# Kernel tuning notes

Hardware: AMD Instinct MI355X
Metric: run time of the kernel (lower is better)

## Reference

```python
import jax, jax.numpy as jnp
import numpy as np

B, T, D, H = 4, 2048, 1024, 16
HD = D // H  # head_dim = 64
SCALE = HD ** -0.5


def setup_inputs() -> dict:
    key = jax.random.key(0)
    k1, k2, k3 = jax.random.split(key, 3)
    x = jax.random.normal(k1, (B, T, D), dtype=jnp.float32)
    # xavier-uniform-like scaling for weights
    qkv_w = jax.random.normal(k2, (3 * D, D), dtype=jnp.float32) * (2.0 / (4 * D)) ** 0.5
    out_w = jax.random.normal(k3, (D, D), dtype=jnp.float32) * (1.0 / D) ** 0.5
    out_b = jnp.zeros((D,), dtype=jnp.float32)
    return {"x": x, "qkv_w": qkv_w, "out_w": out_w, "out_b": out_b}


def reference(x, qkv_w, out_w, out_b):
    Bx, Tx, _ = x.shape
    # qkv projection (nn.Linear: x @ W^T), no bias
    qkv = jnp.einsum('btd,ed->bte', x, qkv_w)  # [B,T,3D]
    qkv = qkv.reshape(Bx, Tx, 3, H, HD).transpose(2, 0, 3, 1, 4)  # [3,B,H,T,hd]
    q, k, v = qkv[0], qkv[1], qkv[2]
    scores = jnp.einsum('bhqd,bhkd->bhqk', q, k) * SCALE  # [B,H,T,T]
    causal = jnp.triu(jnp.ones((Tx, Tx), dtype=bool), k=1)
    scores = jnp.where(causal, -jnp.inf, scores)
    weights = jax.nn.softmax(scores, axis=-1)
    out = jnp.einsum('bhqk,bhkd->bhqd', weights, v)  # [B,H,T,hd]
    out = out.transpose(0, 2, 1, 3).reshape(Bx, Tx, D)
    return jnp.einsum('btd,ed->bte', out, out_w) + out_b
```

## Files before the change

### kernel.cpp

```cpp
#include <hip/hip_runtime.h>
#include <stdint.h>


typedef __bf16 bfx8 __attribute__((ext_vector_type(8)));
typedef float f32x4 __attribute__((ext_vector_type(4)));
typedef float f32x16 __attribute__((ext_vector_type(16)));

__device__ __forceinline__ uint16_t f2b(float f) {
  uint32_t u = __float_as_uint(f);
  u += 0x7fff + ((u >> 16) & 1);
  return (uint16_t)(u >> 16);
}

__device__ __forceinline__ uint32_t cvt_pk(float lo, float hi) {
  uint32_t r;
  asm("v_cvt_pk_bf16_f32 %0, %1, %2" : "=v"(r) : "v"(lo), "v"(hi));
  return r;
}

__device__ __forceinline__ void gld16(const void* g, void* l) {
  __builtin_amdgcn_global_load_lds((const __attribute__((address_space(1))) void*)g,
                                   (__attribute__((address_space(3))) void*)l,
                                   16, 0, 0);
}

__global__ __launch_bounds__(256) void cvt_bf16(const float* __restrict__ in,
                                                uint16_t* __restrict__ out, int n8) {
  int i = blockIdx.x * 256 + threadIdx.x;
  if (i >= n8) return;
  float4 a = ((const float4*)in)[2 * i];
  float4 b = ((const float4*)in)[2 * i + 1];
  union { uint16_t u[8]; uint4 v; } pk;
  pk.u[0] = f2b(a.x); pk.u[1] = f2b(a.y); pk.u[2] = f2b(a.z); pk.u[3] = f2b(a.w);
  pk.u[4] = f2b(b.x); pk.u[5] = f2b(b.y); pk.u[6] = f2b(b.z); pk.u[7] = f2b(b.w);
  ((uint4*)out)[i] = pk.v;
}

template <int OUTF32>
__global__ __launch_bounds__(256) void gemm_bt(const uint16_t* __restrict__ A,
                                               const uint16_t* __restrict__ B,
                                               void* __restrict__ Cout,
                                               const float* __restrict__ bias,
                                               int M, int N, int K, int nbx, int nwg) {
  __shared__ alignas(16) uint16_t As[2][128 * 32];
  __shared__ alignas(16) uint16_t Bs[2][128 * 32];

  int did = blockIdx.x;
  int wg = (did & 7) * (nwg >> 3) + (did >> 3);
  int bx = wg % nbx, by = wg / nbx;
  int m0 = by * 128, n0 = bx * 128;

  int tid = threadIdx.x;
  int lane = tid & 63, wid = tid >> 6;
  int wm = wid >> 1, wn = wid & 1;

  int rs = wid * 16 + (lane >> 2);
  int cs = (lane & 3) * 8;

  f32x4 acc[4][4] = {};

  auto stage = [&](int buf, int kt) {
    int k0 = kt * 32;
    gld16(&A[(size_t)(m0 + rs) * K + k0 + cs],      &As[buf][wid * 512]);
    gld16(&A[(size_t)(m0 + rs + 64) * K + k0 + cs], &As[buf][wid * 512 + 2048]);
    gld16(&B[(size_t)(n0 + rs) * K + k0 + cs],      &Bs[buf][wid * 512]);
    gld16(&B[(size_t)(n0 + rs + 64) * K + k0 + cs], &Bs[buf][wid * 512 + 2048]);
  };

  stage(0, 0);
  __syncthreads();

  int nk = K >> 5;
  int cur = 0;
  int ko = (lane >> 4) * 8;
  for (int kt = 0; kt < nk; ++kt) {
    if (kt + 1 < nk) stage(cur ^ 1, kt + 1);
    bfx8 a[4], b[4];
#pragma unroll
    for (int mi = 0; mi < 4; ++mi)
      a[mi] = *(const bfx8*)&As[cur][(wm * 64 + mi * 16 + (lane & 15)) * 32 + ko];
#pragma unroll
    for (int ni = 0; ni < 4; ++ni)
      b[ni] = *(const bfx8*)&Bs[cur][(wn * 64 + ni * 16 + (lane & 15)) * 32 + ko];
#pragma unroll
    for (int mi = 0; mi < 4; ++mi)
#pragma unroll
      for (int ni = 0; ni < 4; ++ni)
        acc[mi][ni] =
            __builtin_amdgcn_mfma_f32_16x16x32_bf16(a[mi], b[ni], acc[mi][ni], 0, 0, 0);
    __syncthreads();
    cur ^= 1;
  }

#pragma unroll
  for (int mi = 0; mi < 4; ++mi) {
    int row = m0 + wm * 64 + mi * 16 + ((lane >> 4) << 2);
#pragma unroll
    for (int ni = 0; ni < 4; ++ni) {
      int col = n0 + wn * 64 + ni * 16 + (lane & 15);
#pragma unroll
      for (int r = 0; r < 4; ++r) {
        float v = acc[mi][ni][r];
        if (OUTF32)
          ((float*)Cout)[(size_t)(row + r) * N + col] = v + bias[col];
        else
          ((uint16_t*)Cout)[(size_t)(row + r) * N + col] = f2b(v);
      }
    }
  }
}

__global__ __launch_bounds__(256, 2) void flash_attn(const uint16_t* __restrict__ qkv,
                                                     uint16_t* __restrict__ attnb) {
  const int T = 2048, D3 = 3072;
  const float CSC = 0.125f * 1.44269504f;
  __shared__ alignas(16) uint16_t Ks[3][64 * 64];
  __shared__ alignas(16) uint16_t Vt[3][64 * 64];

  int d = blockIdx.x;
  int bh = d & 63;
  int a = d >> 6;
  int b = bh >> 4, h = bh & 15;

  int tid = threadIdx.x, lane = tid & 63, wid = tid >> 6;
  int l31 = lane & 31, hi = lane >> 5;
  int swz = (lane & 7) << 3;

  size_t base = (size_t)b * T * D3;
  int hoff = h * 64;
  const uint16_t* kbase = &qkv[base + 1024 + hoff];
  const uint16_t* vbase = &qkv[base + 2048 + hoff];

  int krow = wid * 16 + (lane >> 3);
  int kc = ((lane & 7) << 3) ^ ((krow & 7) << 3);
  int vr = (tid & 31) * 2;
  int vc = (tid >> 5) * 8;

  for (int p = 0; p < 2; ++p) {
    int qb = (p == 0) ? (15 - a) : a;
    int q0 = qb << 7;
    int qw = q0 + wid * 32;
    int ntile = 2 * qb + 2;

    float mC = -1e30f, l_r = 0.f;
    f32x16 acc0 = {}, acc1 = {};
    bfx8 pf[4];
    int smax_prev = -1, vb_prev = 0;

    bfx8 qf[4];
    {
      const uint16_t* qp = &qkv[base + (size_t)(qw + l31) * D3 + hoff + 8 * hi];
#pragma unroll
      for (int h4 = 0; h4 < 4; ++h4) qf[h4] = *(const bfx8*)(qp + 16 * h4);
    }

    uint4 vA0, vA1, vB0, vB1;

    auto loadV = [&](int kv0, uint4& r0, uint4& r1) {
      r0 = *(const uint4*)&vbase[(size_t)(kv0 + vr) * D3 + vc];
      r1 = *(const uint4*)&vbase[(size_t)(kv0 + vr + 1) * D3 + vc];
    };
    auto stageK = [&](int buf, int kv0) {
      gld16(&kbase[(size_t)(kv0 + krow) * D3 + kc], &Ks[buf][wid * 1024]);
      gld16(&kbase[(size_t)(kv0 + krow + 8) * D3 + kc], &Ks[buf][wid * 1024 + 512]);
    };
    auto writeV = [&](int vb, const uint4& r0, const uint4& r1) {
      union { uint4 v; uint16_t u[8]; } x, y;
      x.v = r0; y.v = r1;
#pragma unroll
      for (int j = 0; j < 8; ++j) {
        int hd = vc + j;
        uint32_t pk = (uint32_t)x.u[j] | ((uint32_t)y.u[j] << 16);
        *(uint32_t*)&Vt[vb][hd * 64 + (vr ^ ((hd & 7) << 3))] = pk;
      }
    };
    auto doPV = [&]() {
      const uint16_t* vp = &Vt[vb_prev][0];
      __builtin_amdgcn_s_setprio(1);
#pragma unroll
      for (int s = 0; s < 4; ++s) {
        if (s <= smax_prev) {
          bfx8 v0 = *(const bfx8*)&vp[l31 * 64 + ((16 * s + 8 * hi) ^ swz)];
          acc0 = __builtin_amdgcn_mfma_f32_32x32x16_bf16(v0, pf[s], acc0, 0, 0, 0);
          bfx8 v1 = *(const bfx8*)&vp[(32 + l31) * 64 + ((16 * s + 8 * hi) ^ swz)];
          acc1 = __builtin_amdgcn_mfma_f32_32x32x16_bf16(v1, pf[s], acc1, 0, 0, 0);
        }
      }
      __builtin_amdgcn_s_setprio(0);
    };

    loadV(0, vA0, vA1);
    stageK(0, 0);
    writeV(0, vA0, vA1);
    loadV(64, vB0, vB1);
    stageK(1, 64);
    asm volatile("s_waitcnt vmcnt(0) lgkmcnt(0)" ::: "memory");
    __builtin_amdgcn_s_barrier();
    __builtin_amdgcn_sched_barrier(0);

    auto subiter = [&](int t, uint4& f0, uint4& f1, uint4& c0, uint4& c1) {
      int kv0 = t << 6;
      bool issue = (t + 2 < ntile);
      if (issue) {
        loadV((t + 2) << 6, f0, f1);
        stageK((t + 2) % 3, (t + 2) << 6);
      }
      bool active = (kv0 <= qw);
      int tmax = (qw > kv0) ? 2 : 1;
      f32x16 st0 = {}, st1 = {};
      if (active) {
        const uint16_t* kp = &Ks[t % 3][0];
        __builtin_amdgcn_s_setprio(1);
#pragma unroll
        for (int h4 = 0; h4 < 4; ++h4) {
          bfx8 kf0 = *(const bfx8*)&kp[l31 * 64 + ((16 * h4 + 8 * hi) ^ swz)];
          st0 = __builtin_amdgcn_mfma_f32_32x32x16_bf16(kf0, qf[h4], st0, 0, 0, 0);
          if (tmax == 2) {
            bfx8 kf1 = *(const bfx8*)&kp[(32 + l31) * 64 + ((16 * h4 + 8 * hi) ^ swz)];
            st1 = __builtin_amdgcn_mfma_f32_32x32x16_bf16(kf1, qf[h4], st1, 0, 0, 0);
          }
        }
        __builtin_amdgcn_s_setprio(0);
      }

      if (smax_prev >= 0) { doPV(); smax_prev = -1; }

      if (active) {
        int q = qw + l31;
        float mx0 = -1e30f, mx1 = -1e30f;
        if (kv0 == qw) {
#pragma unroll
          for (int r = 0; r < 16; ++r) {
            int kv = kv0 + (r & 3) + 8 * (r >> 2) + 4 * hi;
            float v = st0[r];
            if (kv > q) v = -1e30f;
            st0[r] = v;
            mx0 = fmaxf(mx0, v);
          }
        } else {
#pragma unroll
          for (int r = 0; r < 16; ++r) mx0 = fmaxf(mx0, st0[r]);
        }
        if (tmax == 2) {
          if (kv0 + 32 == qw) {
#pragma unroll
            for (int r = 0; r < 16; ++r) {
              int kv = kv0 + 32 + (r & 3) + 8 * (r >> 2) + 4 * hi;
              float v = st1[r];
              if (kv > q) v = -1e30f;
              st1[r] = v;
              mx1 = fmaxf(mx1, v);
            }
          } else {
#pragma unroll
            for (int r = 0; r < 16; ++r) mx1 = fmaxf(mx1, st1[r]);
          }
        }
        float mS = fmaxf(mx0, mx1) * CSC;
        if (!__all(mS - mC <= 8.0f)) {
          float mSp = fmaxf(mS, __shfl_xor(mS, 32));
          float mCn = fmaxf(mC, mSp);
          float fac = __builtin_amdgcn_exp2f(mC - mCn);
          mC = mCn;
          l_r *= fac;
          acc0 *= fac;
          acc1 *= fac;
        }
        float l0 = 0.f, l1 = 0.f, l2 = 0.f, l3 = 0.f;
#pragma unroll
        for (int r = 0; r < 16; r += 4) {
          float e0 = __builtin_amdgcn_exp2f(fmaf(st0[r], CSC, -mC));
          float e1 = __builtin_amdgcn_exp2f(fmaf(st0[r + 1], CSC, -mC));
          float e2 = __builtin_amdgcn_exp2f(fmaf(st0[r + 2], CSC, -mC));
          float e3 = __builtin_amdgcn_exp2f(fmaf(st0[r + 3], CSC, -mC));
          st0[r] = e0; st0[r + 1] = e1; st0[r + 2] = e2; st0[r + 3] = e3;
          l0 += e0; l1 += e1; l2 += e2; l3 += e3;
        }
        if (tmax == 2) {
#pragma unroll
          for (int r = 0; r < 16; r += 4) {
            float e0 = __builtin_amdgcn_exp2f(fmaf(st1[r], CSC, -mC));
            float e1 = __builtin_amdgcn_exp2f(fmaf(st1[r + 1], CSC, -mC));
            float e2 = __builtin_amdgcn_exp2f(fmaf(st1[r + 2], CSC, -mC));
            float e3 = __builtin_amdgcn_exp2f(fmaf(st1[r + 3], CSC, -mC));
            st1[r] = e0; st1[r + 1] = e1; st1[r + 2] = e2; st1[r + 3] = e3;
            l0 += e0; l1 += e1; l2 += e2; l3 += e3;
          }
        }
        l_r += (l0 + l1) + (l2 + l3);

        int smax = (qw + 31 - kv0) >> 4;
        if (smax > 3) smax = 3;
#pragma unroll
        for (int s = 0; s < 4; ++s) {
          if (s <= smax) {
            int pb = 8 * (s & 1);
            uint32_t W0, W1, W2, W3;
            if (s < 2) {
              W0 = cvt_pk(st0[pb + 0], st0[pb + 1]);
              W1 = cvt_pk(st0[pb + 2], st0[pb + 3]);
              W2 = cvt_pk(st0[pb + 4], st0[pb + 5]);
              W3 = cvt_pk(st0[pb + 6], st0[pb + 7]);
            } else {
              W0 = cvt_pk(st1[pb + 0], st1[pb + 1]);
              W1 = cvt_pk(st1[pb + 2], st1[pb + 3]);
              W2 = cvt_pk(st1[pb + 4], st1[pb + 5]);
              W3 = cvt_pk(st1[pb + 6], st1[pb + 7]);
            }
            auto rA = __builtin_amdgcn_permlane32_swap(W0, W2, false, false);
            auto rB = __builtin_amdgcn_permlane32_swap(W1, W3, false, false);
            union { uint32_t u[4]; bfx8 v; } pk;
            pk.u[0] = rA[0]; pk.u[1] = rB[0]; pk.u[2] = rA[1]; pk.u[3] = rB[1];
            pf[s] = pk.v;
          }
        }
        smax_prev = smax;
        vb_prev = t % 3;
      }

      if (t + 1 < ntile) writeV((t + 1) % 3, c0, c1);

      if (issue)
        asm volatile("s_waitcnt vmcnt(4) lgkmcnt(0)" ::: "memory");
      else
        asm volatile("s_waitcnt vmcnt(0) lgkmcnt(0)" ::: "memory");
      __builtin_amdgcn_s_barrier();
      __builtin_amdgcn_sched_barrier(0);
    };

    for (int t = 0; t < ntile; t += 2) {
      subiter(t, vA0, vA1, vB0, vB1);
      subiter(t + 1, vB0, vB1, vA0, vA1);
    }
    if (smax_prev >= 0) doPV();

    float l_tot = l_r + __shfl_xor(l_r, 32);
    __syncthreads();
    uint16_t* ow = ((uint16_t*)Ks) + wid * 2048;
    float rl = 1.0f / l_tot;
#pragma unroll
    for (int f = 0; f < 2; ++f) {
#pragma unroll
      for (int r = 0; r < 16; r += 2) {
        int hd = 32 * f + (r & 3) + 8 * (r >> 2) + 4 * hi;
        float v0 = (f ? acc1[r] : acc0[r]) * rl;
        float v1 = (f ? acc1[r + 1] : acc0[r + 1]) * rl;
        *(uint32_t*)&ow[l31 * 64 + (hd ^ ((l31 & 7) << 3))] = cvt_pk(v0, v1);
      }
    }
    int row = lane >> 1, cb = (lane & 1) * 32;
    int q = q0 + wid * 32 + row;
    int rs = (row & 7) << 3;
    uint16_t* dst = &attnb[(size_t)(b * T + q) * 1024 + hoff + cb];
#pragma unroll
    for (int cc = 0; cc < 4; ++cc)
      *(uint4*)&dst[cc * 8] = *(const uint4*)&ow[row * 64 + ((cb + cc * 8) ^ rs)];
    __syncthreads();
  }
}

extern "C" void kernel_launch(void* const* d_in, const int* in_sizes, int n_in,
                              void* d_out, int out_size, void* d_ws, size_t ws_size,
                              hipStream_t stream) {
  const float* x = (const float*)d_in[0];
  const float* qkv_w = (const float*)d_in[1];
  const float* out_w = (const float*)d_in[2];
  const float* out_b = (const float*)d_in[3];
  float* out = (float*)d_out;

  char* ws = (char*)d_ws;
  uint16_t* xb    = (uint16_t*)(ws);
  uint16_t* qkvb  = (uint16_t*)(ws + 16777216);
  uint16_t* attnb = (uint16_t*)(ws + 67108864);
  uint16_t* wqkvb = (uint16_t*)(ws + 83886080);
  uint16_t* wob   = (uint16_t*)(ws + 90177536);

  cvt_bf16<<<4096, 256, 0, stream>>>(x, xb, 1048576);
  cvt_bf16<<<1536, 256, 0, stream>>>(qkv_w, wqkvb, 393216);
  cvt_bf16<<<512, 256, 0, stream>>>(out_w, wob, 131072);

  gemm_bt<0><<<1536, 256, 0, stream>>>(xb, wqkvb, (void*)qkvb, nullptr,
                                       8192, 3072, 1024, 24, 1536);
  flash_attn<<<512, 256, 0, stream>>>(qkvb, attnb);
  gemm_bt<1><<<512, 256, 0, stream>>>(attnb, wob, (void*)out, out_b,
                                      8192, 1024, 1024, 8, 512);
}
```

Baseline: 193.9 us.

## Rebalance causal attention work across 768 blocks and fuse fp32-to-bf16 conversions

The flash attention grid changes from 512 blocks that each handle a long and a short query block pair to 768 blocks. One third take a single heavy query block (15-tr), one third take a single mid-heavy block (8+tr), and one third take two light blocks. Occupancy hint rises to 3 blocks per CU. This is meant to even out per-block causal work and raise wave concurrency on the GPU. The three conversion launches are also merged into one kernel to save launch overhead. Higher occupancy may constrain registers and add spills.

```diff
diff --git a/kernel.cpp b/kernel.cpp
--- a/kernel.cpp
+++ b/kernel.cpp
@@ -24,10 +24,18 @@
                                    16, 0, 0);
 }
 
-__global__ __launch_bounds__(256) void cvt_bf16(const float* __restrict__ in,
-                                                uint16_t* __restrict__ out, int n8) {
+__global__ __launch_bounds__(256) void cvt_all(const float* __restrict__ x,
+                                               const float* __restrict__ w1,
+                                               const float* __restrict__ w2,
+                                               uint16_t* __restrict__ xb,
+                                               uint16_t* __restrict__ w1b,
+                                               uint16_t* __restrict__ w2b) {
   int i = blockIdx.x * 256 + threadIdx.x;
-  if (i >= n8) return;
+  const float* in;
+  uint16_t* out;
+  if (i < 1048576) { in = x; out = xb; }
+  else if (i < 1048576 + 393216) { in = w1; out = w1b; i -= 1048576; }
+  else { in = w2; out = w2b; i -= 1048576 + 393216; }
   float4 a = ((const float4*)in)[2 * i];
   float4 b = ((const float4*)in)[2 * i + 1];
   union { uint16_t u[8]; uint4 v; } pk;
@@ -110,16 +118,17 @@
   }
 }
 
-__global__ __launch_bounds__(256, 2) void flash_attn(const uint16_t* __restrict__ qkv,
+__global__ __launch_bounds__(256, 3) void flash_attn(const uint16_t* __restrict__ qkv,
                                                      uint16_t* __restrict__ attnb) {
   const int T = 2048, D3 = 3072;
   const float CSC = 0.125f * 1.44269504f;
   __shared__ alignas(16) uint16_t Ks[3][64 * 64];
   __shared__ alignas(16) uint16_t Vt[3][64 * 64];
 
-  int d = blockIdx.x;
-  int bh = d & 63;
-  int a = d >> 6;
+  int did = blockIdx.x;
+  int c = did & 255;
+  int j = did >> 8;
+  int bh = c >> 2, tr = c & 3;
   int b = bh >> 4, h = bh & 15;
 
   int tid = threadIdx.x, lane = tid & 63, wid = tid >> 6;
@@ -136,8 +145,9 @@
   int vr = (tid & 31) * 2;
   int vc = (tid >> 5) * 8;
 
-  for (int p = 0; p < 2; ++p) {
-    int qb = (p == 0) ? (15 - a) : a;
+  int nparts = (j == 2) ? 2 : 1;
+  for (int p = 0; p < nparts; ++p) {
+    int qb = (j == 0) ? (15 - tr) : (j == 1) ? (8 + tr) : ((p == 0) ? (7 - tr) : tr);
     int q0 = qb << 7;
     int qw = q0 + wid * 32;
     int ntile = 2 * qb + 2;
@@ -168,9 +178,9 @@
       union { uint4 v; uint16_t u[8]; } x, y;
       x.v = r0; y.v = r1;
 #pragma unroll
-      for (int j = 0; j < 8; ++j) {
-        int hd = vc + j;
-        uint32_t pk = (uint32_t)x.u[j] | ((uint32_t)y.u[j] << 16);
+      for (int jj = 0; jj < 8; ++jj) {
+        int hd = vc + jj;
+        uint32_t pk = (uint32_t)x.u[jj] | ((uint32_t)y.u[jj] << 16);
         *(uint32_t*)&Vt[vb][hd * 64 + (vr ^ ((hd & 7) << 3))] = pk;
       }
     };
@@ -375,13 +385,11 @@
   uint16_t* wqkvb = (uint16_t*)(ws + 83886080);
   uint16_t* wob   = (uint16_t*)(ws + 90177536);
 
-  cvt_bf16<<<4096, 256, 0, stream>>>(x, xb, 1048576);
-  cvt_bf16<<<1536, 256, 0, stream>>>(qkv_w, wqkvb, 393216);
-  cvt_bf16<<<512, 256, 0, stream>>>(out_w, wob, 131072);
+  cvt_all<<<6144, 256, 0, stream>>>(x, qkv_w, out_w, xb, wqkvb, wob);
 
   gemm_bt<0><<<1536, 256, 0, stream>>>(xb, wqkvb, (void*)qkvb, nullptr,
                                        8192, 3072, 1024, 24, 1536);
-  flash_attn<<<512, 256, 0, stream>>>(qkvb, attnb);
+  flash_attn<<<768, 256, 0, stream>>>(qkvb, attnb);
   gemm_bt<1><<<512, 256, 0, stream>>>(attnb, wob, (void*)out, out_b,
                                       8192, 1024, 1024, 8, 512);
 }
```

After: 241.5 us. 1.25x slower.
